# Performance work log

Hardware: AMD Instinct MI355X
Metric: run time of the kernel (lower is better)

Reference implementation:

```python
import jax, jax.numpy as jnp
import numpy as np

EPS = 1e-5  # BatchNorm eps

def _gcn_norm(edge_index, edge_weight, n):
    # PyG gcn_norm with add_self_loops=True, fill_value=1.0
    loop = jnp.arange(n, dtype=edge_index.dtype)
    row = jnp.concatenate([edge_index[0], loop])
    col = jnp.concatenate([edge_index[1], loop])
    ew = jnp.concatenate([edge_weight, jnp.ones((n,), edge_weight.dtype)])
    deg = jax.ops.segment_sum(ew, col, num_segments=n)
    dis = jnp.where(deg > 0, jax.lax.rsqrt(jnp.maximum(deg, 1e-30)), 0.0)
    norm = dis[row] * ew * dis[col]
    return row, col, norm

def _gcn_conv(x, W, b, row, col, norm, n):
    h = x @ W                               # [N, out]
    msg = h[row] * norm[:, None]            # gather + edge scale
    out = jax.ops.segment_sum(msg, col, num_segments=n)
    return out + b

def _bn_eval(x, gamma, beta, mean, var):
    return (x - mean) * jax.lax.rsqrt(var + EPS) * gamma + beta

def setup_inputs() -> dict:
    key = jax.random.key(0)
    ks = jax.random.split(key, 12)
    N, E, V, H = 100000, 1600000, 256, 128
    x = jax.random.normal(ks[0], (N, V), jnp.float32)
    edge_index = jax.random.randint(ks[1], (2, E), 0, N, jnp.int64)
    edge_weight = jax.random.uniform(ks[2], (E,), jnp.float32)
    s = lambda fan: 1.0 / np.sqrt(fan)
    return {
        "x": x, "edge_index": edge_index, "edge_weight": edge_weight,
        "W1": jax.random.normal(ks[3], (V, H), jnp.float32) * s(V),
        "b1": jnp.zeros((H,), jnp.float32),
        "W2": jax.random.normal(ks[4], (H, H), jnp.float32) * s(H),
        "b2": jnp.zeros((H,), jnp.float32),
        "W3": jax.random.normal(ks[5], (H, 1), jnp.float32) * s(H),
        "b3": jnp.zeros((1,), jnp.float32),
        "Wres": jax.random.normal(ks[6], (V, H), jnp.float32) * s(V),
        "g1": jnp.ones((H,), jnp.float32), "be1": jnp.zeros((H,), jnp.float32),
        "m1": jax.random.normal(ks[7], (H,), jnp.float32) * 0.01,
        "v1": jnp.ones((H,), jnp.float32),
        "g2": jnp.ones((H,), jnp.float32), "be2": jnp.zeros((H,), jnp.float32),
        "m2": jax.random.normal(ks[8], (H,), jnp.float32) * 0.01,
        "v2": jnp.ones((H,), jnp.float32),
    }

def reference(x, edge_index, edge_weight, W1, b1, W2, b2, W3, b3, Wres,
              g1, be1, m1, v1, g2, be2, m2, v2):
    n = x.shape[0]
    row, col, norm = _gcn_norm(edge_index, edge_weight, n)
    res = x @ Wres                                   # residual branch
    h = _gcn_conv(x, W1, b1, row, col, norm, n)
    h = jax.nn.relu(_bn_eval(h, g1, be1, m1, v1))    # dropout off (eval)
    h = _gcn_conv(h, W2, b2, row, col, norm, n) + res
    h = jax.nn.relu(_bn_eval(h, g2, be2, m2, v2))
    h = _gcn_conv(h, W3, b3, row, col, norm, n)      # [N, 1]
    return jnp.squeeze(h, axis=1)
```

## Files before the change

kernel.cpp:

```cpp
#include <hip/hip_runtime.h>
#include <hip/hip_bf16.h>

#define BN_EPS 1e-5f

using short8 = __attribute__((ext_vector_type(8))) short;
using f32x4  = __attribute__((ext_vector_type(4))) float;

#define FIX_SCALE 262144.0f
#define FIX_MASK  0x01ffffffu
#define CNT_ONE   (1u << 25)

static __device__ __forceinline__ unsigned short f2bf(float f) {
  unsigned int u = __float_as_uint(f);
  unsigned int r = (u + 0x7fffu + ((u >> 16) & 1u)) >> 16;
  return (unsigned short)r;
}


static __global__ void cast_weights(const float* __restrict__ W1, const float* __restrict__ Wres,
                                    const float* __restrict__ W2,
                                    unsigned short* __restrict__ B2,
                                    unsigned short* __restrict__ BT2) {
  int i = blockIdx.x * blockDim.x + threadIdx.x;
  if (i < 256 * 256) {
    int n = i >> 8, k = i & 255;
    float v = (n < 128) ? W1[k * 128 + n] : Wres[k * 128 + (n - 128)];
    B2[(k >> 5) * 8192 + n * 32 + (k & 31)] = f2bf(v);
  } else if (i < 256 * 256 + 128 * 128) {
    int j = i - 256 * 256;
    int n = j >> 7, k = j & 127;
    BT2[j] = f2bf(W2[k * 128 + n]);
  }
}


static __global__ __launch_bounds__(256)
void hist_kernel(const int* __restrict__ col, const float* __restrict__ ew,
                 unsigned int* __restrict__ packed,
                 unsigned short* __restrict__ rank, int E, int N) {
  unsigned int xcc;
  asm volatile("s_getreg_b32 %0, hwreg(HW_REG_XCC_ID)" : "=s"(xcc));
  xcc &= 7u;
  unsigned int* mytab = packed + (size_t)xcc * N;
  int base = blockIdx.x * (256 * 4) + threadIdx.x;
#pragma unroll
  for (int j = 0; j < 4; ++j) {
    int e = base + j * 256;
    if (e < E) {
      int c = col[e];
      unsigned int fx = (unsigned int)(ew[e] * FIX_SCALE + 0.5f);
      unsigned int old = __hip_atomic_fetch_add(&mytab[c], CNT_ONE | fx,
                                                __ATOMIC_RELAXED,
                                                __HIP_MEMORY_SCOPE_WORKGROUP);
      rank[e] = (unsigned short)(((old >> 25) & 0x1fffu) | (xcc << 13));
    }
  }
}


static __global__ __launch_bounds__(256)
void gemm1_kernel(const float* __restrict__ A, const unsigned short* __restrict__ B2,
                  unsigned short* __restrict__ C0, unsigned short* __restrict__ C1, int M) {
  __shared__ unsigned short As[2 * 64 * 40];

  int t = threadIdx.x;
  int wv = t >> 6, lane = t & 63;
  int quad = lane >> 4, l15 = lane & 15;
  int m0 = blockIdx.x * 64;

  f32x4 acc[4][4];
#pragma unroll
  for (int i = 0; i < 4; ++i)
#pragma unroll
    for (int j = 0; j < 4; ++j) acc[i][j] = (f32x4){0.f, 0.f, 0.f, 0.f};

  int ar = t >> 2;
  int ac = (t & 3) * 8;
  bool avalid = (m0 + ar) < M;
  const float* Arow = A + (size_t)(m0 + ar) * 256 + ac;
  const unsigned short* Bfrag = B2 + (wv * 64 + l15) * 32 + quad * 8;

  float4 a0 = make_float4(0.f, 0.f, 0.f, 0.f), a1 = a0;
  if (avalid) {
    a0 = *(const float4*)(Arow + 0);
    a1 = *(const float4*)(Arow + 4);
  }
  {
    short8 av;
    av[0] = (short)f2bf(a0.x); av[1] = (short)f2bf(a0.y);
    av[2] = (short)f2bf(a0.z); av[3] = (short)f2bf(a0.w);
    av[4] = (short)f2bf(a1.x); av[5] = (short)f2bf(a1.y);
    av[6] = (short)f2bf(a1.z); av[7] = (short)f2bf(a1.w);
    *(short8*)&As[ar * 40 + ac] = av;
  }
  short8 bc[4];
#pragma unroll
  for (int nt = 0; nt < 4; ++nt)
    bc[nt] = *(const short8*)(Bfrag + nt * 512);
  __syncthreads();

#pragma unroll 2
  for (int s = 0; s < 8; ++s) {
    int cur = (s & 1) ? 2560 : 0;

    short8 bn[4];
    if (s < 7) {
#pragma unroll
      for (int nt = 0; nt < 4; ++nt)
        bn[nt] = *(const short8*)(Bfrag + (s + 1) * 8192 + nt * 512);
      if (avalid) {
        a0 = *(const float4*)(Arow + (s + 1) * 32);
        a1 = *(const float4*)(Arow + (s + 1) * 32 + 4);
      }
    }

    short8 af[4];
#pragma unroll
    for (int mt = 0; mt < 4; ++mt)
      af[mt] = *(const short8*)&As[cur + (mt * 16 + l15) * 40 + quad * 8];
#pragma unroll
    for (int mt = 0; mt < 4; ++mt)
#pragma unroll
      for (int nt = 0; nt < 4; ++nt)
        acc[mt][nt] = __builtin_amdgcn_mfma_f32_16x16x32_bf16(af[mt], bc[nt], acc[mt][nt], 0, 0, 0);

    if (s < 7) {
      short8 av;
      av[0] = (short)f2bf(a0.x); av[1] = (short)f2bf(a0.y);
      av[2] = (short)f2bf(a0.z); av[3] = (short)f2bf(a0.w);
      av[4] = (short)f2bf(a1.x); av[5] = (short)f2bf(a1.y);
      av[6] = (short)f2bf(a1.z); av[7] = (short)f2bf(a1.w);
      *(short8*)&As[(cur ^ 2560) + ar * 40 + ac] = av;
#pragma unroll
      for (int nt = 0; nt < 4; ++nt) bc[nt] = bn[nt];
    }
    __syncthreads();
  }

  int nbase = wv * 64;
#pragma unroll
  for (int mt = 0; mt < 4; ++mt) {
#pragma unroll
    for (int nt = 0; nt < 4; ++nt) {
      int n = nbase + nt * 16 + l15;
#pragma unroll
      for (int reg = 0; reg < 4; ++reg) {
        size_t m = (size_t)(m0 + mt * 16 + quad * 4 + reg);
        if (nbase < 128) C0[m * 128 + n] = f2bf(acc[mt][nt][reg]);
        else             C1[m * 128 + (n - 128)] = f2bf(acc[mt][nt][reg]);
      }
    }
  }
}


#define SCAN_B 256
#define SCAN_I 16
static __global__ void scanA(const unsigned int* __restrict__ packed,
                             float* __restrict__ dis, int* __restrict__ cnt,
                             int* __restrict__ startV, int* __restrict__ blkSum, int N) {
  __shared__ int sh[SCAN_B];
  int t = threadIdx.x;
  int vbase = blockIdx.x * (SCAN_B * SCAN_I) + t * SCAN_I;
  int v[SCAN_I];
  int tot = 0;
#pragma unroll
  for (int g = 0; g < 2; ++g) {
    int c = (vbase >> 3) + g;
    int csum = 0;
    if (c < N) {
      unsigned int usum = 0;
#pragma unroll
      for (int r = 0; r < 8; ++r) {
        unsigned int pv = packed[(size_t)r * N + c];
        int cr = (int)(pv >> 25);
        v[g * 8 + r] = cr;
        csum += cr;
        usum += (pv & FIX_MASK);
      }
      cnt[c] = csum;
      dis[c] = rsqrtf(1.0f + (float)usum * (1.0f / FIX_SCALE));
    } else {
#pragma unroll
      for (int r = 0; r < 8; ++r) v[g * 8 + r] = 0;
    }
    tot += csum;
  }
  sh[t] = tot;
  __syncthreads();
  int self = tot;
  for (int off = 1; off < SCAN_B; off <<= 1) {
    int add = (t >= off) ? sh[t - off] : 0;
    __syncthreads();
    sh[t] += add;
    __syncthreads();
  }
  int excl = sh[t] - self;
  if (t == SCAN_B - 1) blkSum[blockIdx.x] = sh[t];
  int run = excl;
#pragma unroll
  for (int j = 0; j < SCAN_I; ++j) {
    if (vbase + j < 8 * N) startV[vbase + j] = run;
    run += v[j];
  }
}

static __global__ void scanB(const int* __restrict__ blkSum, int* __restrict__ blkOff, int nb) {
  __shared__ int sh[256];
  int t = threadIdx.x;
  int v = (t < nb) ? blkSum[t] : 0;
  sh[t] = v;
  __syncthreads();
  for (int off = 1; off < 256; off <<= 1) {
    int add = (t >= off) ? sh[t - off] : 0;
    __syncthreads();
    sh[t] += add;
    __syncthreads();
  }
  if (t < nb) blkOff[t] = sh[t] - v;
}

static __global__ void scanC(int* startV, const int* __restrict__ blkOff, int NV) {
  int i = blockIdx.x * blockDim.x + threadIdx.x;
  if (i < NV) startV[i] += blkOff[i / (SCAN_B * SCAN_I)];
}

static __global__ void place_kernel(const int* __restrict__ row, const int* __restrict__ col,
                                    const float* __restrict__ ew, const float* __restrict__ dis,
                                    const int* __restrict__ startV,
                                    const unsigned short* __restrict__ rank,
                                    long long* __restrict__ edges, int E) {
  int e = blockIdx.x * blockDim.x + threadIdx.x;
  if (e < E) {
    int r = row[e], c = col[e];
    unsigned int rk = rank[e];
    int pos = startV[c * 8 + (rk >> 13)] + (int)(rk & 0x1fffu);
    float nrm = dis[r] * ew[e];
    long long v = ((long long)__float_as_int(nrm) << 32) | (unsigned int)r;
    __builtin_nontemporal_store(v, &edges[pos]);
  }
}


static __global__ __launch_bounds__(256)
void gemm2_mfma(const unsigned short* __restrict__ A, const unsigned short* __restrict__ BT,
                unsigned short* __restrict__ C) {
  __shared__ unsigned short As[128 * 40];
  __shared__ unsigned short Bs[128 * 40];
  int t = threadIdx.x;
  int wv = t >> 6, lane = t & 63;
  int quad = lane >> 4, l15 = lane & 15;
  int m0 = blockIdx.x * 128;

  f32x4 acc[4][4];
#pragma unroll
  for (int i = 0; i < 4; ++i)
#pragma unroll
    for (int j = 0; j < 4; ++j) acc[i][j] = (f32x4){0.f, 0.f, 0.f, 0.f};

  int sr = t >> 1, sc = (t & 1) * 16;

  for (int k0 = 0; k0 < 128; k0 += 32) {
    short8 a0 = *(const short8*)(A + (size_t)(m0 + sr) * 128 + k0 + sc);
    short8 a1 = *(const short8*)(A + (size_t)(m0 + sr) * 128 + k0 + sc + 8);
    *(short8*)&As[sr * 40 + sc]     = a0;
    *(short8*)&As[sr * 40 + sc + 8] = a1;
    short8 b0 = *(const short8*)(BT + (size_t)sr * 128 + k0 + sc);
    short8 b1 = *(const short8*)(BT + (size_t)sr * 128 + k0 + sc + 8);
    *(short8*)&Bs[sr * 40 + sc]     = b0;
    *(short8*)&Bs[sr * 40 + sc + 8] = b1;
    __syncthreads();

    int mb = (wv >> 1) * 64, nb = (wv & 1) * 64;
    short8 af[4], bf[4];
#pragma unroll
    for (int mt = 0; mt < 4; ++mt)
      af[mt] = *(const short8*)&As[(mb + mt * 16 + l15) * 40 + quad * 8];
#pragma unroll
    for (int nt = 0; nt < 4; ++nt)
      bf[nt] = *(const short8*)&Bs[(nb + nt * 16 + l15) * 40 + quad * 8];
#pragma unroll
    for (int mt = 0; mt < 4; ++mt)
#pragma unroll
      for (int nt = 0; nt < 4; ++nt)
        acc[mt][nt] = __builtin_amdgcn_mfma_f32_16x16x32_bf16(af[mt], bf[nt], acc[mt][nt], 0, 0, 0);
    __syncthreads();
  }

  int mb = (wv >> 1) * 64, nb = (wv & 1) * 64;
#pragma unroll
  for (int mt = 0; mt < 4; ++mt)
#pragma unroll
    for (int nt = 0; nt < 4; ++nt) {
      int n = nb + nt * 16 + l15;
#pragma unroll
      for (int reg = 0; reg < 4; ++reg) {
        size_t m = (size_t)(m0 + mb + mt * 16 + quad * 4 + reg);
        C[m * 128 + n] = f2bf(acc[mt][nt][reg]);
      }
    }
}


#define PROP_GATHER_BODY                                                        \
  int c0 = lane * 2;                                                            \
  float d = dis[w];                                                             \
  float acc0, acc1;                                                             \
  {                                                                             \
    unsigned int u = Hsrc[(size_t)w * 64 + lane];                               \
    acc0 = d * __uint_as_float(u << 16);                                        \
    acc1 = d * __uint_as_float(u & 0xffff0000u);                                \
  }                                                                             \
  int s = start8[(size_t)w * 8], n = cnt[w];                                    \
  int k = 0;                                                                    \
  while (k < n) {                                                               \
    int chunk = min(n - k, 64);                                                 \
    int idx = 0;                                                                \
    float wt = 0.f;                                                             \
    if (lane < chunk) {                                                         \
      long long ev = edges[s + k + lane];                                       \
      idx = (int)(unsigned int)(ev & 0xffffffffLL);                             \
      wt  = __int_as_float((int)(ev >> 32));                                    \
    }                                                                           \
    for (int j = 0; j < chunk; j += 8) {                                        \
      int   i0 = __shfl(idx, j + 0, 64), i1 = __shfl(idx, j + 1, 64);           \
      int   i2 = __shfl(idx, j + 2, 64), i3 = __shfl(idx, j + 3, 64);           \
      int   i4 = __shfl(idx, j + 4, 64), i5 = __shfl(idx, j + 5, 64);           \
      int   i6 = __shfl(idx, j + 6, 64), i7 = __shfl(idx, j + 7, 64);           \
      float w0 = __shfl(wt, j + 0, 64), w1 = __shfl(wt, j + 1, 64);             \
      float w2 = __shfl(wt, j + 2, 64), w3 = __shfl(wt, j + 3, 64);             \
      float w4 = __shfl(wt, j + 4, 64), w5 = __shfl(wt, j + 5, 64);             \
      float w6 = __shfl(wt, j + 6, 64), w7 = __shfl(wt, j + 7, 64);             \
      unsigned int u0 = Hsrc[(size_t)i0 * 64 + lane];                           \
      unsigned int u1 = Hsrc[(size_t)i1 * 64 + lane];                           \
      unsigned int u2 = Hsrc[(size_t)i2 * 64 + lane];                           \
      unsigned int u3 = Hsrc[(size_t)i3 * 64 + lane];                           \
      unsigned int u4 = Hsrc[(size_t)i4 * 64 + lane];                           \
      unsigned int u5 = Hsrc[(size_t)i5 * 64 + lane];                           \
      unsigned int u6 = Hsrc[(size_t)i6 * 64 + lane];                           \
      unsigned int u7 = Hsrc[(size_t)i7 * 64 + lane];                           \
      acc0 = fmaf(w0, __uint_as_float(u0 << 16), acc0);                         \
      acc1 = fmaf(w0, __uint_as_float(u0 & 0xffff0000u), acc1);                 \
      acc0 = fmaf(w1, __uint_as_float(u1 << 16), acc0);                         \
      acc1 = fmaf(w1, __uint_as_float(u1 & 0xffff0000u), acc1);                 \
      acc0 = fmaf(w2, __uint_as_float(u2 << 16), acc0);                         \
      acc1 = fmaf(w2, __uint_as_float(u2 & 0xffff0000u), acc1);                 \
      acc0 = fmaf(w3, __uint_as_float(u3 << 16), acc0);                         \
      acc1 = fmaf(w3, __uint_as_float(u3 & 0xffff0000u), acc1);                 \
      acc0 = fmaf(w4, __uint_as_float(u4 << 16), acc0);                         \
      acc1 = fmaf(w4, __uint_as_float(u4 & 0xffff0000u), acc1);                 \
      acc0 = fmaf(w5, __uint_as_float(u5 << 16), acc0);                         \
      acc1 = fmaf(w5, __uint_as_float(u5 & 0xffff0000u), acc1);                 \
      acc0 = fmaf(w6, __uint_as_float(u6 << 16), acc0);                         \
      acc1 = fmaf(w6, __uint_as_float(u6 & 0xffff0000u), acc1);                 \
      acc0 = fmaf(w7, __uint_as_float(u7 << 16), acc0);                         \
      acc1 = fmaf(w7, __uint_as_float(u7 & 0xffff0000u), acc1);                 \
    }                                                                           \
    k += chunk;                                                                 \
  }                                                                             \
  acc0 *= d;                                                                    \
  acc1 *= d;

static __global__ __launch_bounds__(256)
void prop128_bf16out(const unsigned int* __restrict__ Hsrc,
                     const int* __restrict__ start8, const int* __restrict__ cnt,
                     const long long* __restrict__ edges,
                     const float* __restrict__ dis,
                     const float* __restrict__ bvec,
                     const float* __restrict__ g, const float* __restrict__ be,
                     const float* __restrict__ mean, const float* __restrict__ var,
                     unsigned int* __restrict__ Outb, int N) {
  int w = (int)((blockIdx.x * blockDim.x + threadIdx.x) >> 6);
  int lane = threadIdx.x & 63;
  if (w >= N) return;
  PROP_GATHER_BODY
  float x0 = acc0 + bvec[c0];
  float x1 = acc1 + bvec[c0 + 1];
  float s0 = g[c0] * rsqrtf(var[c0] + BN_EPS);
  float s1 = g[c0 + 1] * rsqrtf(var[c0 + 1] + BN_EPS);
  x0 = fmaxf((x0 - mean[c0]) * s0 + be[c0], 0.f);
  x1 = fmaxf((x1 - mean[c0 + 1]) * s1 + be[c0 + 1], 0.f);
  unsigned int packed = (unsigned int)f2bf(x0) | ((unsigned int)f2bf(x1) << 16);
  Outb[(size_t)w * 64 + lane] = packed;
}

static __global__ __launch_bounds__(256)
void prop128_w3out(const unsigned int* __restrict__ Hsrc,
                   const int* __restrict__ start8, const int* __restrict__ cnt,
                   const long long* __restrict__ edges,
                   const float* __restrict__ dis,
                   const float* __restrict__ bvec,
                   const float* __restrict__ g, const float* __restrict__ be,
                   const float* __restrict__ mean, const float* __restrict__ var,
                   const unsigned int* __restrict__ resb, const float* __restrict__ W3,
                   float* __restrict__ h3, int N) {
  int w = (int)((blockIdx.x * blockDim.x + threadIdx.x) >> 6);
  int lane = threadIdx.x & 63;
  if (w >= N) return;
  PROP_GATHER_BODY
  unsigned int ru = resb[(size_t)w * 64 + lane];
  float x0 = acc0 + bvec[c0]     + __uint_as_float(ru << 16);
  float x1 = acc1 + bvec[c0 + 1] + __uint_as_float(ru & 0xffff0000u);
  float s0 = g[c0] * rsqrtf(var[c0] + BN_EPS);
  float s1 = g[c0 + 1] * rsqrtf(var[c0 + 1] + BN_EPS);
  x0 = fmaxf((x0 - mean[c0]) * s0 + be[c0], 0.f);
  x1 = fmaxf((x1 - mean[c0 + 1]) * s1 + be[c0 + 1], 0.f);
  float v = x0 * W3[c0] + x1 * W3[c0 + 1];
#pragma unroll
  for (int off = 32; off > 0; off >>= 1) v += __shfl_down(v, off, 64);
  if (lane == 0) h3[w] = v;
}


static __global__ void prop3_kernel(const float* __restrict__ h3,
                                    const int* __restrict__ start8, const int* __restrict__ cnt,
                                    const long long* __restrict__ edges,
                                    const float* __restrict__ dis, const float* __restrict__ b3,
                                    float* __restrict__ out, int N) {
  int i = blockIdx.x * blockDim.x + threadIdx.x;
  if (i >= N) return;
  float d = dis[i];
  float acc = d * h3[i];
  int s = start8[(size_t)i * 8], n = cnt[i];
  for (int k = 0; k < n; ++k) {
    long long ev = edges[s + k];
    int src = (int)(unsigned int)(ev & 0xffffffffLL);
    float wt = __int_as_float((int)(ev >> 32));
    acc = fmaf(wt, h3[src], acc);
  }
  out[i] = acc * d + b3[0];
}


extern "C" void kernel_launch(void* const* d_in, const int* in_sizes, int n_in,
                              void* d_out, int out_size, void* d_ws, size_t ws_size,
                              hipStream_t stream) {
  const float* x    = (const float*)d_in[0];
  const int*   ei   = (const int*)d_in[1];
  const float* ew   = (const float*)d_in[2];
  const float* W1   = (const float*)d_in[3];
  const float* b1   = (const float*)d_in[4];
  const float* W2   = (const float*)d_in[5];
  const float* b2   = (const float*)d_in[6];
  const float* W3   = (const float*)d_in[7];
  const float* b3   = (const float*)d_in[8];
  const float* Wres = (const float*)d_in[9];
  const float* g1   = (const float*)d_in[10];
  const float* be1  = (const float*)d_in[11];
  const float* m1   = (const float*)d_in[12];
  const float* v1   = (const float*)d_in[13];
  const float* g2   = (const float*)d_in[14];
  const float* be2  = (const float*)d_in[15];
  const float* m2   = (const float*)d_in[16];
  const float* v2   = (const float*)d_in[17];

  int Hh = in_sizes[4];
  int V  = in_sizes[3] / Hh;
  int N  = in_sizes[0] / V;
  int E  = in_sizes[2];
  const int* row = ei;
  const int* col = ei + E;

  int Mp = ((N + 127) / 128) * 128;

  char* p = (char*)d_ws;
  auto alloc = [&](size_t bytes) -> char* {
    char* r = p;
    p += (bytes + 255) & ~(size_t)255;
    return r;
  };
  unsigned int* packed = (unsigned int*)alloc((size_t)N * 8 * 4);
  float* dis    = (float*)alloc((size_t)N * 4);
  int*   cnt    = (int*)  alloc((size_t)N * 4);
  int*   startV = (int*)  alloc((size_t)N * 8 * 4);
  int*   blkSum = (int*)  alloc(256 * 4);
  int*   blkOff = (int*)  alloc(256 * 4);
  unsigned short* rank = (unsigned short*)alloc((size_t)E * 2);
  long long* edges = (long long*)alloc((size_t)E * 8);
  float* h3     = (float*)alloc((size_t)N * 4);
  unsigned short* B2  = (unsigned short*)alloc((size_t)256 * 256 * 2);
  unsigned short* BT2 = (unsigned short*)alloc((size_t)128 * 128 * 2);
  unsigned short* bufG  = (unsigned short*)alloc((size_t)Mp * 128 * 2);
  unsigned short* bufH1 = (unsigned short*)alloc((size_t)Mp * 128 * 2);
  unsigned short* bufRes = (unsigned short*)alloc((size_t)Mp * 128 * 2);
  (void)ws_size; (void)n_in; (void)out_size;

  int TB = 256;
  hipMemsetAsync(packed, 0, (size_t)N * 8 * 4, stream);
  cast_weights<<<(256 * 256 + 128 * 128 + TB - 1) / TB, TB, 0, stream>>>(W1, Wres, W2, B2, BT2);

  int hB = (E + TB * 4 - 1) / (TB * 4);
  hist_kernel<<<hB, TB, 0, stream>>>(col, ew, packed, rank, E, N);
  gemm1_kernel<<<Mp / 64, TB, 0, stream>>>(x, B2, bufG, bufRes, N);

  int NV = 8 * N;
  int nb = (NV + SCAN_B * SCAN_I - 1) / (SCAN_B * SCAN_I);
  scanA<<<nb, SCAN_B, 0, stream>>>(packed, dis, cnt, startV, blkSum, N);
  scanB<<<1, 256, 0, stream>>>(blkSum, blkOff, nb);
  scanC<<<(NV + TB - 1) / TB, TB, 0, stream>>>(startV, blkOff, NV);
  place_kernel<<<(E + TB - 1) / TB, TB, 0, stream>>>(row, col, ew, dis, startV,
                                                     rank, edges, E);

  int propBlocks = (int)(((size_t)N * 64 + TB - 1) / TB);
  prop128_bf16out<<<propBlocks, TB, 0, stream>>>((const unsigned int*)bufG, startV, cnt,
                                                 edges, dis, b1, g1, be1, m1, v1,
                                                 (unsigned int*)bufH1, N);

  gemm2_mfma<<<Mp / 128, 256, 0, stream>>>(bufH1, BT2, bufG);

  prop128_w3out<<<propBlocks, TB, 0, stream>>>((const unsigned int*)bufG, startV, cnt,
                                               edges, dis, b2, g2, be2, m2, v2,
                                               (const unsigned int*)bufRes, W3, h3, N);

  prop3_kernel<<<(N + TB - 1) / TB, TB, 0, stream>>>(h3, startV, cnt, edges,
                                                     dis, b3, (float*)d_out, N);
}
```

Baseline: 508.4 us.

## Split feature matrices into 16-column groups for cache-local sparse gathers

Measured after the change: 940.9 us. 85.1% more time.

```diff
diff --git a/kernel.cpp b/kernel.cpp
--- a/kernel.cpp
+++ b/kernel.cpp
@@ -9,6 +9,7 @@
 #define FIX_SCALE 262144.0f
 #define FIX_MASK  0x01ffffffu
 #define CNT_ONE   (1u << 25)
+
 
 static __device__ __forceinline__ unsigned short f2bf(float f) {
   unsigned int u = __float_as_uint(f);
@@ -33,7 +34,6 @@
   }
 }
 
-
 static __global__ __launch_bounds__(256)
 void hist_kernel(const int* __restrict__ col, const float* __restrict__ ew,
                  unsigned int* __restrict__ packed,
@@ -60,7 +60,8 @@
 
 static __global__ __launch_bounds__(256)
 void gemm1_kernel(const float* __restrict__ A, const unsigned short* __restrict__ B2,
-                  unsigned short* __restrict__ C0, unsigned short* __restrict__ C1, int M) {
+                  unsigned short* __restrict__ C0, unsigned short* __restrict__ C1,
+                  int M, int Mp) {
   __shared__ unsigned short As[2 * 64 * 40];
 
   int t = threadIdx.x;
@@ -143,11 +144,13 @@
 #pragma unroll
     for (int nt = 0; nt < 4; ++nt) {
       int n = nbase + nt * 16 + l15;
+      int nn = (n < 128) ? n : n - 128;
+      unsigned short* Cd = (n < 128) ? C0 : C1;
+      size_t grp = (size_t)(nn >> 4) * Mp;
 #pragma unroll
       for (int reg = 0; reg < 4; ++reg) {
         size_t m = (size_t)(m0 + mt * 16 + quad * 4 + reg);
-        if (nbase < 128) C0[m * 128 + n] = f2bf(acc[mt][nt][reg]);
-        else             C1[m * 128 + (n - 128)] = f2bf(acc[mt][nt][reg]);
+        Cd[(grp + m) * 16 + (nn & 15)] = f2bf(acc[mt][nt][reg]);
       }
     }
   }
@@ -244,7 +247,7 @@
 
 static __global__ __launch_bounds__(256)
 void gemm2_mfma(const unsigned short* __restrict__ A, const unsigned short* __restrict__ BT,
-                unsigned short* __restrict__ C) {
+                unsigned short* __restrict__ C, int Mp) {
   __shared__ unsigned short As[128 * 40];
   __shared__ unsigned short Bs[128 * 40];
   int t = threadIdx.x;
@@ -261,8 +264,9 @@
   int sr = t >> 1, sc = (t & 1) * 16;
 
   for (int k0 = 0; k0 < 128; k0 += 32) {
-    short8 a0 = *(const short8*)(A + (size_t)(m0 + sr) * 128 + k0 + sc);
-    short8 a1 = *(const short8*)(A + (size_t)(m0 + sr) * 128 + k0 + sc + 8);
+    const unsigned short* Ar = A + ((size_t)((k0 + sc) >> 4) * Mp + (m0 + sr)) * 16;
+    short8 a0 = *(const short8*)(Ar);
+    short8 a1 = *(const short8*)(Ar + 8);
     *(short8*)&As[sr * 40 + sc]     = a0;
     *(short8*)&As[sr * 40 + sc + 8] = a1;
     short8 b0 = *(const short8*)(BT + (size_t)sr * 128 + k0 + sc);
@@ -293,122 +297,151 @@
 #pragma unroll
     for (int nt = 0; nt < 4; ++nt) {
       int n = nb + nt * 16 + l15;
+      size_t grp = (size_t)(n >> 4) * Mp;
 #pragma unroll
       for (int reg = 0; reg < 4; ++reg) {
         size_t m = (size_t)(m0 + mb + mt * 16 + quad * 4 + reg);
-        C[m * 128 + n] = f2bf(acc[mt][nt][reg]);
+        C[(grp + m) * 16 + (n & 15)] = f2bf(acc[mt][nt][reg]);
       }
     }
 }
 
 
-#define PROP_GATHER_BODY                                                        \
-  int c0 = lane * 2;                                                            \
-  float d = dis[w];                                                             \
-  float acc0, acc1;                                                             \
-  {                                                                             \
-    unsigned int u = Hsrc[(size_t)w * 64 + lane];                               \
-    acc0 = d * __uint_as_float(u << 16);                                        \
-    acc1 = d * __uint_as_float(u & 0xffff0000u);                                \
-  }                                                                             \
-  int s = start8[(size_t)w * 8], n = cnt[w];                                    \
-  int k = 0;                                                                    \
-  while (k < n) {                                                               \
-    int chunk = min(n - k, 64);                                                 \
-    int idx = 0;                                                                \
-    float wt = 0.f;                                                             \
-    if (lane < chunk) {                                                         \
-      long long ev = edges[s + k + lane];                                       \
-      idx = (int)(unsigned int)(ev & 0xffffffffLL);                             \
-      wt  = __int_as_float((int)(ev >> 32));                                    \
-    }                                                                           \
-    for (int j = 0; j < chunk; j += 8) {                                        \
-      int   i0 = __shfl(idx, j + 0, 64), i1 = __shfl(idx, j + 1, 64);           \
-      int   i2 = __shfl(idx, j + 2, 64), i3 = __shfl(idx, j + 3, 64);           \
-      int   i4 = __shfl(idx, j + 4, 64), i5 = __shfl(idx, j + 5, 64);           \
-      int   i6 = __shfl(idx, j + 6, 64), i7 = __shfl(idx, j + 7, 64);           \
-      float w0 = __shfl(wt, j + 0, 64), w1 = __shfl(wt, j + 1, 64);             \
-      float w2 = __shfl(wt, j + 2, 64), w3 = __shfl(wt, j + 3, 64);             \
-      float w4 = __shfl(wt, j + 4, 64), w5 = __shfl(wt, j + 5, 64);             \
-      float w6 = __shfl(wt, j + 6, 64), w7 = __shfl(wt, j + 7, 64);             \
-      unsigned int u0 = Hsrc[(size_t)i0 * 64 + lane];                           \
-      unsigned int u1 = Hsrc[(size_t)i1 * 64 + lane];                           \
-      unsigned int u2 = Hsrc[(size_t)i2 * 64 + lane];                           \
-      unsigned int u3 = Hsrc[(size_t)i3 * 64 + lane];                           \
-      unsigned int u4 = Hsrc[(size_t)i4 * 64 + lane];                           \
-      unsigned int u5 = Hsrc[(size_t)i5 * 64 + lane];                           \
-      unsigned int u6 = Hsrc[(size_t)i6 * 64 + lane];                           \
-      unsigned int u7 = Hsrc[(size_t)i7 * 64 + lane];                           \
-      acc0 = fmaf(w0, __uint_as_float(u0 << 16), acc0);                         \
-      acc1 = fmaf(w0, __uint_as_float(u0 & 0xffff0000u), acc1);                 \
-      acc0 = fmaf(w1, __uint_as_float(u1 << 16), acc0);                         \
-      acc1 = fmaf(w1, __uint_as_float(u1 & 0xffff0000u), acc1);                 \
-      acc0 = fmaf(w2, __uint_as_float(u2 << 16), acc0);                         \
-      acc1 = fmaf(w2, __uint_as_float(u2 & 0xffff0000u), acc1);                 \
-      acc0 = fmaf(w3, __uint_as_float(u3 << 16), acc0);                         \
-      acc1 = fmaf(w3, __uint_as_float(u3 & 0xffff0000u), acc1);                 \
-      acc0 = fmaf(w4, __uint_as_float(u4 << 16), acc0);                         \
-      acc1 = fmaf(w4, __uint_as_float(u4 & 0xffff0000u), acc1);                 \
-      acc0 = fmaf(w5, __uint_as_float(u5 << 16), acc0);                         \
-      acc1 = fmaf(w5, __uint_as_float(u5 & 0xffff0000u), acc1);                 \
-      acc0 = fmaf(w6, __uint_as_float(u6 << 16), acc0);                         \
-      acc1 = fmaf(w6, __uint_as_float(u6 & 0xffff0000u), acc1);                 \
-      acc0 = fmaf(w7, __uint_as_float(u7 << 16), acc0);                         \
-      acc1 = fmaf(w7, __uint_as_float(u7 & 0xffff0000u), acc1);                 \
-    }                                                                           \
-    k += chunk;                                                                 \
-  }                                                                             \
-  acc0 *= d;                                                                    \
-  acc1 *= d;
-
 static __global__ __launch_bounds__(256)
-void prop128_bf16out(const unsigned int* __restrict__ Hsrc,
-                     const int* __restrict__ start8, const int* __restrict__ cnt,
-                     const long long* __restrict__ edges,
-                     const float* __restrict__ dis,
-                     const float* __restrict__ bvec,
-                     const float* __restrict__ g, const float* __restrict__ be,
-                     const float* __restrict__ mean, const float* __restrict__ var,
-                     unsigned int* __restrict__ Outb, int N) {
-  int w = (int)((blockIdx.x * blockDim.x + threadIdx.x) >> 6);
-  int lane = threadIdx.x & 63;
-  if (w >= N) return;
-  PROP_GATHER_BODY
-  float x0 = acc0 + bvec[c0];
-  float x1 = acc1 + bvec[c0 + 1];
-  float s0 = g[c0] * rsqrtf(var[c0] + BN_EPS);
-  float s1 = g[c0 + 1] * rsqrtf(var[c0 + 1] + BN_EPS);
-  x0 = fmaxf((x0 - mean[c0]) * s0 + be[c0], 0.f);
-  x1 = fmaxf((x1 - mean[c0 + 1]) * s1 + be[c0 + 1], 0.f);
-  unsigned int packed = (unsigned int)f2bf(x0) | ((unsigned int)f2bf(x1) << 16);
-  Outb[(size_t)w * 64 + lane] = packed;
+void prop1_split(const unsigned int* __restrict__ Hg,
+                 const int* __restrict__ startV, const int* __restrict__ cnt,
+                 const long long* __restrict__ edges,
+                 const float* __restrict__ dis,
+                 const float* __restrict__ bvec,
+                 const float* __restrict__ gam, const float* __restrict__ bet,
+                 const float* __restrict__ mean, const float* __restrict__ var,
+                 unsigned int* __restrict__ Og, int N, int Mp) {
+  int g = blockIdx.x & 7;
+  int base = (blockIdx.x >> 3) * 16;
+  int wv = threadIdx.x >> 6, lane = threadIdx.x & 63;
+  int sub = lane >> 3, w = lane & 7;
+  const unsigned int* H = Hg + (size_t)g * Mp * 8;
+  unsigned int* O = Og + (size_t)g * Mp * 8;
+  int c0 = g * 16 + w * 2;
+  float s0 = gam[c0] * rsqrtf(var[c0] + BN_EPS);
+  float s1 = gam[c0 + 1] * rsqrtf(var[c0 + 1] + BN_EPS);
+  float mn0 = mean[c0], mn1 = mean[c0 + 1];
+  float bt0 = bet[c0], bt1 = bet[c0 + 1];
+  float bb0 = bvec[c0], bb1 = bvec[c0 + 1];
+
+#pragma unroll
+  for (int i = 0; i < 4; ++i) {
+    int dst = base + wv * 4 + i;
+    if (dst >= N) break;
+    float d = dis[dst];
+    float a0 = 0.f, a1 = 0.f;
+    if (sub == 0) {
+      unsigned int u = H[(size_t)dst * 8 + w];
+      a0 = d * __uint_as_float(u << 16);
+      a1 = d * __uint_as_float(u & 0xffff0000u);
+    }
+    int s = startV[(size_t)dst * 8], n = cnt[dst];
+    int k = sub;
+    long long ev = (k < n) ? edges[s + k] : 0;
+    while (k < n) {
+      int kn = k + 8;
+      long long evn = (kn < n) ? edges[s + kn] : 0;
+      int idx = (int)(unsigned int)(ev & 0xffffffffLL);
+      float wt = __int_as_float((int)(ev >> 32));
+      unsigned int u = H[(size_t)idx * 8 + w];
+      a0 = fmaf(wt, __uint_as_float(u << 16), a0);
+      a1 = fmaf(wt, __uint_as_float(u & 0xffff0000u), a1);
+      ev = evn; k = kn;
+    }
+    a0 += __shfl_xor(a0, 8, 64);  a1 += __shfl_xor(a1, 8, 64);
+    a0 += __shfl_xor(a0, 16, 64); a1 += __shfl_xor(a1, 16, 64);
+    a0 += __shfl_xor(a0, 32, 64); a1 += __shfl_xor(a1, 32, 64);
+    if (sub == 0) {
+      float x0 = a0 * d + bb0;
+      float x1 = a1 * d + bb1;
+      x0 = fmaxf((x0 - mn0) * s0 + bt0, 0.f);
+      x1 = fmaxf((x1 - mn1) * s1 + bt1, 0.f);
+      O[(size_t)dst * 8 + w] = (unsigned int)f2bf(x0) | ((unsigned int)f2bf(x1) << 16);
+    }
+  }
 }
 
 static __global__ __launch_bounds__(256)
-void prop128_w3out(const unsigned int* __restrict__ Hsrc,
-                   const int* __restrict__ start8, const int* __restrict__ cnt,
-                   const long long* __restrict__ edges,
-                   const float* __restrict__ dis,
-                   const float* __restrict__ bvec,
-                   const float* __restrict__ g, const float* __restrict__ be,
-                   const float* __restrict__ mean, const float* __restrict__ var,
-                   const unsigned int* __restrict__ resb, const float* __restrict__ W3,
-                   float* __restrict__ h3, int N) {
-  int w = (int)((blockIdx.x * blockDim.x + threadIdx.x) >> 6);
-  int lane = threadIdx.x & 63;
-  if (w >= N) return;
-  PROP_GATHER_BODY
-  unsigned int ru = resb[(size_t)w * 64 + lane];
-  float x0 = acc0 + bvec[c0]     + __uint_as_float(ru << 16);
-  float x1 = acc1 + bvec[c0 + 1] + __uint_as_float(ru & 0xffff0000u);
-  float s0 = g[c0] * rsqrtf(var[c0] + BN_EPS);
-  float s1 = g[c0 + 1] * rsqrtf(var[c0 + 1] + BN_EPS);
-  x0 = fmaxf((x0 - mean[c0]) * s0 + be[c0], 0.f);
-  x1 = fmaxf((x1 - mean[c0 + 1]) * s1 + be[c0 + 1], 0.f);
-  float v = x0 * W3[c0] + x1 * W3[c0 + 1];
-#pragma unroll
-  for (int off = 32; off > 0; off >>= 1) v += __shfl_down(v, off, 64);
-  if (lane == 0) h3[w] = v;
+void prop2_split(const unsigned int* __restrict__ Hg,
+                 const int* __restrict__ startV, const int* __restrict__ cnt,
+                 const long long* __restrict__ edges,
+                 const float* __restrict__ dis,
+                 const float* __restrict__ bvec,
+                 const float* __restrict__ gam, const float* __restrict__ bet,
+                 const float* __restrict__ mean, const float* __restrict__ var,
+                 const unsigned int* __restrict__ Resg, const float* __restrict__ W3,
+                 float* __restrict__ Hpart, int N, int Mp) {
+  int g = blockIdx.x & 7;
+  int base = (blockIdx.x >> 3) * 16;
+  int wv = threadIdx.x >> 6, lane = threadIdx.x & 63;
+  int sub = lane >> 3, w = lane & 7;
+  const unsigned int* H = Hg + (size_t)g * Mp * 8;
+  const unsigned int* R = Resg + (size_t)g * Mp * 8;
+  int c0 = g * 16 + w * 2;
+  float s0 = gam[c0] * rsqrtf(var[c0] + BN_EPS);
+  float s1 = gam[c0 + 1] * rsqrtf(var[c0 + 1] + BN_EPS);
+  float mn0 = mean[c0], mn1 = mean[c0 + 1];
+  float bt0 = bet[c0], bt1 = bet[c0 + 1];
+  float bb0 = bvec[c0], bb1 = bvec[c0 + 1];
+  float w30 = W3[c0], w31 = W3[c0 + 1];
+
+#pragma unroll
+  for (int i = 0; i < 4; ++i) {
+    int dst = base + wv * 4 + i;
+    if (dst >= N) break;
+    float d = dis[dst];
+    float a0 = 0.f, a1 = 0.f;
+    if (sub == 0) {
+      unsigned int u = H[(size_t)dst * 8 + w];
+      a0 = d * __uint_as_float(u << 16);
+      a1 = d * __uint_as_float(u & 0xffff0000u);
+    }
+    int s = startV[(size_t)dst * 8], n = cnt[dst];
+    int k = sub;
+    long long ev = (k < n) ? edges[s + k] : 0;
+    while (k < n) {
+      int kn = k + 8;
+      long long evn = (kn < n) ? edges[s + kn] : 0;
+      int idx = (int)(unsigned int)(ev & 0xffffffffLL);
+      float wt = __int_as_float((int)(ev >> 32));
+      unsigned int u = H[(size_t)idx * 8 + w];
+      a0 = fmaf(wt, __uint_as_float(u << 16), a0);
+      a1 = fmaf(wt, __uint_as_float(u & 0xffff0000u), a1);
+      ev = evn; k = kn;
+    }
+    a0 += __shfl_xor(a0, 8, 64);  a1 += __shfl_xor(a1, 8, 64);
+    a0 += __shfl_xor(a0, 16, 64); a1 += __shfl_xor(a1, 16, 64);
+    a0 += __shfl_xor(a0, 32, 64); a1 += __shfl_xor(a1, 32, 64);
+    float v = 0.f;
+    if (sub == 0) {
+      unsigned int ru = R[(size_t)dst * 8 + w];
+      float x0 = a0 * d + bb0 + __uint_as_float(ru << 16);
+      float x1 = a1 * d + bb1 + __uint_as_float(ru & 0xffff0000u);
+      x0 = fmaxf((x0 - mn0) * s0 + bt0, 0.f);
+      x1 = fmaxf((x1 - mn1) * s1 + bt1, 0.f);
+      v = x0 * w30 + x1 * w31;
+    }
+    v += __shfl_down(v, 4, 64);
+    v += __shfl_down(v, 2, 64);
+    v += __shfl_down(v, 1, 64);
+    if (lane == 0) Hpart[(size_t)g * Mp + dst] = v;
+  }
+}
+
+static __global__ void reduce_h3(const float* __restrict__ Hpart, float* __restrict__ h3,
+                                 int N, int Mp) {
+  int i = blockIdx.x * blockDim.x + threadIdx.x;
+  if (i < N) {
+    float v = 0.f;
+#pragma unroll
+    for (int g = 0; g < 8; ++g) v += Hpart[(size_t)g * Mp + i];
+    h3[i] = v;
+  }
 }
 
 
@@ -478,6 +511,7 @@
   unsigned short* rank = (unsigned short*)alloc((size_t)E * 2);
   long long* edges = (long long*)alloc((size_t)E * 8);
   float* h3     = (float*)alloc((size_t)N * 4);
+  float* Hpart  = (float*)alloc((size_t)Mp * 8 * 4);
   unsigned short* B2  = (unsigned short*)alloc((size_t)256 * 256 * 2);
   unsigned short* BT2 = (unsigned short*)alloc((size_t)128 * 128 * 2);
   unsigned short* bufG  = (unsigned short*)alloc((size_t)Mp * 128 * 2);
@@ -491,7 +525,7 @@
 
   int hB = (E + TB * 4 - 1) / (TB * 4);
   hist_kernel<<<hB, TB, 0, stream>>>(col, ew, packed, rank, E, N);
-  gemm1_kernel<<<Mp / 64, TB, 0, stream>>>(x, B2, bufG, bufRes, N);
+  gemm1_kernel<<<Mp / 64, TB, 0, stream>>>(x, B2, bufG, bufRes, N, Mp);
 
   int NV = 8 * N;
   int nb = (NV + SCAN_B * SCAN_I - 1) / (SCAN_B * SCAN_I);
@@ -501,16 +535,17 @@
   place_kernel<<<(E + TB - 1) / TB, TB, 0, stream>>>(row, col, ew, dis, startV,
                                                      rank, edges, E);
 
-  int propBlocks = (int)(((size_t)N * 64 + TB - 1) / TB);
-  prop128_bf16out<<<propBlocks, TB, 0, stream>>>((const unsigned int*)bufG, startV, cnt,
-                                                 edges, dis, b1, g1, be1, m1, v1,
-                                                 (unsigned int*)bufH1, N);
-
-  gemm2_mfma<<<Mp / 128, 256, 0, stream>>>(bufH1, BT2, bufG);
-
-  prop128_w3out<<<propBlocks, TB, 0, stream>>>((const unsigned int*)bufG, startV, cnt,
-                                               edges, dis, b2, g2, be2, m2, v2,
-                                               (const unsigned int*)bufRes, W3, h3, N);
+  int pB = 8 * ((N + 15) / 16);
+  prop1_split<<<pB, TB, 0, stream>>>((const unsigned int*)bufG, startV, cnt,
+                                     edges, dis, b1, g1, be1, m1, v1,
+                                     (unsigned int*)bufH1, N, Mp);
+
+  gemm2_mfma<<<Mp / 128, 256, 0, stream>>>(bufH1, BT2, bufG, Mp);
+
+  prop2_split<<<pB, TB, 0, stream>>>((const unsigned int*)bufG, startV, cnt,
+                                     edges, dis, b2, g2, be2, m2, v2,
+                                     (const unsigned int*)bufRes, W3, Hpart, N, Mp);
+  reduce_h3<<<(N + TB - 1) / TB, TB, 0, stream>>>(Hpart, h3, N, Mp);
 
   prop3_kernel<<<(N + TB - 1) / TB, TB, 0, stream>>>(h3, startV, cnt, edges,
                                                      dis, b3, (float*)d_out, N);
```
